# Kernel optimization log

Hardware: AMD Instinct MI355X
Metric: run time of the kernel (lower is better)

## Reference

```python
import jax, jax.numpy as jnp
import numpy as np

# Static config (matches init_kwargs); spatial shapes must be static for jit.
SPATIAL = [(96, 96), (48, 48), (24, 24), (12, 12)]  # (H_l, W_l)
D, NH, NL, NP = 256, 8, 4, 4
DH = D // NH
DFFN = 1024


def _ln(x, g, b):
    m = jnp.mean(x, -1, keepdims=True)
    v = jnp.var(x, -1, keepdims=True)
    return (x - m) * jax.lax.rsqrt(v + 1e-5) * g + b


def _bilinear_sample(v, loc, H, W):
    # v: (N, H*W, D) projected value for one level; loc: (N,Lq,NH,NP,2) in [0,1]
    # Matches grid_sample(align_corners=False, padding_mode='zeros'):
    # pixel coord = loc * size - 0.5, zero outside.
    N = v.shape[0]
    v = v.reshape(N, H, W, NH, DH)
    x = loc[..., 0] * W - 0.5
    y = loc[..., 1] * H - 0.5
    x0 = jnp.floor(x)
    y0 = jnp.floor(y)
    wx = x - x0
    wy = y - y0
    x0i = x0.astype(jnp.int32)
    y0i = y0.astype(jnp.int32)
    b = jnp.arange(N)[:, None, None, None]
    h = jnp.arange(NH)[None, None, :, None]

    def gather(yi, xi):
        valid = (yi >= 0) & (yi < H) & (xi >= 0) & (xi < W)
        s = v[b, jnp.clip(yi, 0, H - 1), jnp.clip(xi, 0, W - 1), h]  # (N,Lq,NH,NP,DH)
        return s * valid[..., None]

    s00 = gather(y0i, x0i)
    s01 = gather(y0i, x0i + 1)
    s10 = gather(y0i + 1, x0i)
    s11 = gather(y0i + 1, x0i + 1)
    return (s00 * ((1 - wy) * (1 - wx))[..., None]
            + s01 * ((1 - wy) * wx)[..., None]
            + s10 * (wy * (1 - wx))[..., None]
            + s11 * (wy * wx)[..., None])  # (N,Lq,NH,NP,DH)


def setup_inputs() -> dict:
    key = jax.random.key(0)
    ks = jax.random.split(key, 16)
    N, Lq = 8, 1024

    def nrm(k, shp, scale=1.0):
        return jax.random.normal(k, shp, dtype=jnp.float32) * scale

    return dict(
        tgt=nrm(ks[0], (N, Lq, D)),
        reference_points=jax.random.uniform(ks[1], (N, Lq, NL, 2), dtype=jnp.float32),
        src0=nrm(ks[2], (N, 96 * 96, 16)),
        src1=nrm(ks[3], (N, 48 * 48, 32)),
        src2=nrm(ks[4], (N, 24 * 24, 16)),
        src3=nrm(ks[5], (N, 12 * 12, 32)),
        Wv0=nrm(ks[6], (16, D), 0.25), bv0=jnp.zeros((D,), jnp.float32),
        Wv1=nrm(ks[7], (32, D), 0.18), bv1=jnp.zeros((D,), jnp.float32),
        Woff=nrm(ks[8], (D, NH * NL * NP * 2), 0.01), boff=nrm(ks[9], (NH * NL * NP * 2,), 0.5),
        Wattn=nrm(ks[10], (D, NH * NL * NP), 0.01), battn=jnp.zeros((NH * NL * NP,), jnp.float32),
        Wout=nrm(ks[11], (D, D), 1.0 / 16), bout=jnp.zeros((D,), jnp.float32),
        g1=jnp.ones((D,), jnp.float32), be1=jnp.zeros((D,), jnp.float32),
        W1=nrm(ks[12], (D, DFFN), 1.0 / 16), b1=jnp.zeros((DFFN,), jnp.float32),
        W2=nrm(ks[13], (DFFN, D), 1.0 / 32), b2=jnp.zeros((D,), jnp.float32),
        g3=jnp.ones((D,), jnp.float32), be3=jnp.zeros((D,), jnp.float32),
    )


def reference(tgt, reference_points, src0, src1, src2, src3,
              Wv0, bv0, Wv1, bv1, Woff, boff, Wattn, battn, Wout, bout,
              g1, be1, W1, b1, W2, b2, g3, be3):
    N, Lq, _ = tgt.shape
    # Per-level value projection (value_{idx % (n_levels//2)}: 16->D, 32->D cycling)
    values = [src0 @ Wv0 + bv0, src1 @ Wv1 + bv1, src2 @ Wv0 + bv0, src3 @ Wv1 + bv1]

    off = (tgt @ Woff + boff).reshape(N, Lq, NH, NL, NP, 2)
    attn = jax.nn.softmax((tgt @ Wattn + battn).reshape(N, Lq, NH, NL * NP), axis=-1)
    attn = attn.reshape(N, Lq, NH, NL, NP)

    # offset_normalizer = [W_l, H_l]
    norm = jnp.array([[w, h] for (h, w) in SPATIAL], dtype=tgt.dtype)  # (NL,2)
    loc = reference_points[:, :, None, :, None, :] + off / norm[None, None, None, :, None, :]

    sampled = jnp.stack(
        [_bilinear_sample(values[l], loc[:, :, :, l], SPATIAL[l][0], SPATIAL[l][1])
         for l in range(NL)], axis=3)  # (N,Lq,NH,NL,NP,DH)
    ms_out = jnp.sum(sampled * attn[..., None], axis=(3, 4)).reshape(N, Lq, D)
    ms_out = ms_out @ Wout + bout

    # decoder layer: residual + LN, FFN + residual + LN (dropout=0 / eval)
    t = _ln(tgt + ms_out, g1, be1)
    ff = jax.nn.relu(t @ W1 + b1) @ W2 + b2
    return _ln(t + ff, g3, be3)
```

## Files before the change

kernel.cpp:

```cpp
#include <hip/hip_runtime.h>
#include <math.h>


typedef __bf16 bf16x8 __attribute__((ext_vector_type(8)));
typedef float  f32x4  __attribute__((ext_vector_type(4)));
typedef unsigned short ushort8 __attribute__((ext_vector_type(8)));

#define VB0 0
#define VB1 18874368
#define VB2 23592960
#define VB3 24772608
#define VTOT 25067520

__device__ __forceinline__ unsigned short f2bf(float f) {
    unsigned u = __float_as_uint(f);
    u += 0x7FFF + ((u >> 16) & 1);
    return (unsigned short)(u >> 16);
}

__device__ __forceinline__ void gload16(const void* g, void* l) {
    __builtin_amdgcn_global_load_lds(
        (const __attribute__((address_space(1))) unsigned int*)g,
        (__attribute__((address_space(3))) unsigned int*)l, 16, 0, 0);
}

__global__ __launch_bounds__(256) void prep_kernel(
    const float* __restrict__ tgt, const float* __restrict__ Woff,
    const float* __restrict__ Wattn, const float* __restrict__ Wout,
    const float* __restrict__ W1, const float* __restrict__ W2,
    const float* __restrict__ boff, const float* __restrict__ battn,
    const float* __restrict__ Wv0, const float* __restrict__ Wv1,
    unsigned short* __restrict__ tgt_bf, unsigned short* __restrict__ Btoa,
    unsigned short* __restrict__ WoT, unsigned short* __restrict__ W1T,
    unsigned short* __restrict__ W2T, float* __restrict__ boa,
    unsigned short* __restrict__ WvT0, unsigned short* __restrict__ WvT1)
{
    __shared__ float sT[64][65];
    const int b = blockIdx.x, t = threadIdx.x;
    if (b < 2048) {
        const int i = (b * 256 + t) * 4;
        const float4 v = *(const float4*)&tgt[i];
        ushort4 o;
        o.x = f2bf(v.x); o.y = f2bf(v.y); o.z = f2bf(v.z); o.w = f2bf(v.w);
        *(ushort4*)&tgt_bf[i] = o;
        return;
    }
    if (b == 2048) {
        if (t < 384) boa[t] = (t < 256) ? boff[t] : battn[t - 256];
#pragma unroll
        for (int k = 0; k < 16; ++k) {
            WvT0[t * 32 + k]      = f2bf(Wv0[k * 256 + t]);
            WvT0[t * 32 + 16 + k] = 0;
        }
#pragma unroll
        for (int k = 0; k < 32; ++k)
            WvT1[t * 32 + k] = f2bf(Wv1[k * 256 + t]);
        return;
    }
    int tb = b - 2049;
    const float* src; unsigned short* dst; int srcN, dstK, tn, tk;
    if (tb < 16)       { src = Woff;  dst = Btoa;          srcN = 256;  dstK = 256;  tn = tb >> 2; tk = tb & 3; }
    else if (tb < 24)  { tb -= 16; src = Wattn; dst = Btoa + 65536; srcN = 128; dstK = 256; tn = tb >> 2; tk = tb & 3; }
    else if (tb < 40)  { tb -= 24; src = Wout;  dst = WoT; srcN = 256;  dstK = 256;  tn = tb >> 2; tk = tb & 3; }
    else if (tb < 104) { tb -= 40; src = W1;    dst = W1T; srcN = 1024; dstK = 256;  tn = tb >> 2; tk = tb & 3; }
    else               { tb -= 104; src = W2;   dst = W2T; srcN = 256;  dstK = 1024; tn = tb >> 4; tk = tb & 15; }
    const int n0 = tn * 64, k0 = tk * 64;
    const int j = t & 63, i0 = t >> 6;
#pragma unroll
    for (int s = 0; s < 16; ++s) {
        const int i = i0 + s * 4;
        sT[i][j] = src[(size_t)(k0 + i) * srcN + n0 + j];
    }
    __syncthreads();
#pragma unroll
    for (int s = 0; s < 16; ++s) {
        const int nr = i0 + s * 4;
        dst[(size_t)(n0 + nr) * dstK + k0 + j] = f2bf(sT[j][nr]);
    }
}

template <int BM, int BN, int RELU, int OUTBF16>
__global__ __launch_bounds__(256) void gemm_bf16(
    const unsigned short* __restrict__ A, const unsigned short* __restrict__ Bt,
    const float* __restrict__ bias, float* __restrict__ C32,
    unsigned short* __restrict__ C16, int M, int N, int K)
{
    constexpr int MF = BM / 32, NF = BN / 32;
    constexpr int CA = BM / 16, CB = BN / 16;
    constexpr int CPW = (CA + CB) / 4;

    __shared__ unsigned short As[2][BM * 32];
    __shared__ unsigned short Bs[2][BN * 32];

    const int t = threadIdx.x, wv = t >> 6, l = t & 63;
    const int m0 = blockIdx.y * BM, n0 = blockIdx.x * BN;
    const int wm = wv >> 1, wn = wv & 1;
    const int lr = l >> 2, sl = l & 3;
    const int swsl = sl ^ ((lr >> 1) & 3);
    const int fr = l & 15, kg = l >> 4;
    const int rsw = (fr >> 1) & 3;

    f32x4 acc[MF][NF];
#pragma unroll
    for (int i = 0; i < MF; ++i)
#pragma unroll
        for (int j = 0; j < NF; ++j) acc[i][j] = (f32x4){0.f, 0.f, 0.f, 0.f};

#define STAGE(bufi, k0)                                                        \
    do {                                                                       \
        _Pragma("unroll")                                                      \
        for (int cc = 0; cc < CPW; ++cc) {                                     \
            const int ch = wv * CPW + cc;                                      \
            if (ch < CA) {                                                     \
                gload16(A + (size_t)(m0 + ch * 16 + lr) * K + (k0) + swsl * 8, \
                        &As[bufi][ch * 512]);                                  \
            } else {                                                           \
                const int cb2 = ch - CA;                                       \
                gload16(Bt + (size_t)(n0 + cb2 * 16 + lr) * K + (k0) + swsl * 8,\
                        &Bs[bufi][cb2 * 512]);                                 \
            }                                                                  \
        }                                                                      \
    } while (0)

    const int NT = K >> 5;
    STAGE(0, 0);
    asm volatile("s_waitcnt vmcnt(0)" ::: "memory");
    __syncthreads();

    for (int tt = 0; tt < NT; ++tt) {
        const int cur = tt & 1;
        if (tt + 1 < NT) STAGE(cur ^ 1, (tt + 1) * 32);

        bf16x8 af[MF], bfr[NF];
#pragma unroll
        for (int i = 0; i < MF; ++i)
            af[i] = *(const bf16x8*)&As[cur][(wm * (MF * 16) + i * 16 + fr) * 32 + (kg ^ rsw) * 8];
#pragma unroll
        for (int j = 0; j < NF; ++j)
            bfr[j] = *(const bf16x8*)&Bs[cur][(wn * (NF * 16) + j * 16 + fr) * 32 + (kg ^ rsw) * 8];
#pragma unroll
        for (int i = 0; i < MF; ++i)
#pragma unroll
            for (int j = 0; j < NF; ++j)
                acc[i][j] = __builtin_amdgcn_mfma_f32_16x16x32_bf16(af[i], bfr[j], acc[i][j], 0, 0, 0);

        asm volatile("s_waitcnt vmcnt(0)" ::: "memory");
        __syncthreads();
    }
#undef STAGE

    const int q4 = (l >> 4) * 4;
#pragma unroll
    for (int j = 0; j < NF; ++j) {
        const int col = n0 + wn * (NF * 16) + j * 16 + fr;
        const float bj = bias[col];
#pragma unroll
        for (int i = 0; i < MF; ++i) {
#pragma unroll
            for (int r = 0; r < 4; ++r) {
                const int row = m0 + wm * (MF * 16) + i * 16 + q4 + r;
                float v = acc[i][j][r] + bj;
                if (RELU) v = fmaxf(v, 0.f);
                if (OUTBF16) C16[(size_t)row * N + col] = f2bf(v);
                else         C32[(size_t)row * N + col] = v;
            }
        }
    }
}

__global__ __launch_bounds__(256) void vproj_gemm(
    const float* __restrict__ src0, const float* __restrict__ src1,
    const float* __restrict__ src2, const float* __restrict__ src3,
    const unsigned short* __restrict__ WvT0, const unsigned short* __restrict__ WvT1,
    const float* __restrict__ bv0, const float* __restrict__ bv1,
    unsigned short* __restrict__ vals)
{
    __shared__ unsigned short As[128 * 32];
    __shared__ unsigned short Bs[128 * 32];

    const int ly = blockIdx.y;
    const float* A32; const unsigned short* Bt; const float* bias;
    size_t ob; int lm, Kr;
    if (ly < 576)      { A32 = src0; Bt = WvT0; bias = bv0; ob = VB0; lm = ly;       Kr = 16; }
    else if (ly < 720) { A32 = src1; Bt = WvT1; bias = bv1; ob = VB1; lm = ly - 576; Kr = 32; }
    else if (ly < 756) { A32 = src2; Bt = WvT0; bias = bv0; ob = VB2; lm = ly - 720; Kr = 16; }
    else               { A32 = src3; Bt = WvT1; bias = bv1; ob = VB3; lm = ly - 756; Kr = 32; }

    const int t = threadIdx.x, wv = t >> 6, l = t & 63;
    const int m0 = lm * 128, n0 = blockIdx.x * 128;
    const int wm = wv >> 1, wn = wv & 1;
    const int lr = l >> 2, sl = l & 3;
    const int swsl = sl ^ ((lr >> 1) & 3);
    const int fr = l & 15, kg = l >> 4;
    const int rsw = (fr >> 1) & 3;

#pragma unroll
    for (int cc = 0; cc < 2; ++cc) {
        const int ch = wv * 2 + cc;
        gload16(Bt + (size_t)(n0 + ch * 16 + lr) * 32 + swsl * 8, &Bs[ch * 512]);
    }

    {
        const int r = t >> 1, hh = t & 1;
        const int rs = (r >> 1) & 3;
        if (Kr == 32) {
            const float4* sp = (const float4*)(A32 + (size_t)(m0 + r) * 32 + hh * 16);
            const float4 a0 = sp[0], a1 = sp[1], a2 = sp[2], a3 = sp[3];
            ushort8 w0, w1;
            w0[0] = f2bf(a0.x); w0[1] = f2bf(a0.y); w0[2] = f2bf(a0.z); w0[3] = f2bf(a0.w);
            w0[4] = f2bf(a1.x); w0[5] = f2bf(a1.y); w0[6] = f2bf(a1.z); w0[7] = f2bf(a1.w);
            w1[0] = f2bf(a2.x); w1[1] = f2bf(a2.y); w1[2] = f2bf(a2.z); w1[3] = f2bf(a2.w);
            w1[4] = f2bf(a3.x); w1[5] = f2bf(a3.y); w1[6] = f2bf(a3.z); w1[7] = f2bf(a3.w);
            *(ushort8*)&As[r * 32 + ((hh * 2 + 0) ^ rs) * 8] = w0;
            *(ushort8*)&As[r * 32 + ((hh * 2 + 1) ^ rs) * 8] = w1;
        } else {
            if (hh == 0) {
                const float4* sp = (const float4*)(A32 + (size_t)(m0 + r) * 16);
                const float4 a0 = sp[0], a1 = sp[1], a2 = sp[2], a3 = sp[3];
                ushort8 w0, w1;
                w0[0] = f2bf(a0.x); w0[1] = f2bf(a0.y); w0[2] = f2bf(a0.z); w0[3] = f2bf(a0.w);
                w0[4] = f2bf(a1.x); w0[5] = f2bf(a1.y); w0[6] = f2bf(a1.z); w0[7] = f2bf(a1.w);
                w1[0] = f2bf(a2.x); w1[1] = f2bf(a2.y); w1[2] = f2bf(a2.z); w1[3] = f2bf(a2.w);
                w1[4] = f2bf(a3.x); w1[5] = f2bf(a3.y); w1[6] = f2bf(a3.z); w1[7] = f2bf(a3.w);
                *(ushort8*)&As[r * 32 + ((0) ^ rs) * 8] = w0;
                *(ushort8*)&As[r * 32 + ((1) ^ rs) * 8] = w1;
            } else {
                const ushort8 z = {0, 0, 0, 0, 0, 0, 0, 0};
                *(ushort8*)&As[r * 32 + ((2) ^ rs) * 8] = z;
                *(ushort8*)&As[r * 32 + ((3) ^ rs) * 8] = z;
            }
        }
    }
    asm volatile("s_waitcnt vmcnt(0)" ::: "memory");
    __syncthreads();

    f32x4 acc[4][4];
#pragma unroll
    for (int i = 0; i < 4; ++i)
#pragma unroll
        for (int j = 0; j < 4; ++j) acc[i][j] = (f32x4){0.f, 0.f, 0.f, 0.f};

    bf16x8 af[4], bfr[4];
#pragma unroll
    for (int i = 0; i < 4; ++i)
        af[i] = *(const bf16x8*)&As[(wm * 64 + i * 16 + fr) * 32 + (kg ^ rsw) * 8];
#pragma unroll
    for (int j = 0; j < 4; ++j)
        bfr[j] = *(const bf16x8*)&Bs[(wn * 64 + j * 16 + fr) * 32 + (kg ^ rsw) * 8];
#pragma unroll
    for (int i = 0; i < 4; ++i)
#pragma unroll
        for (int j = 0; j < 4; ++j)
            acc[i][j] = __builtin_amdgcn_mfma_f32_16x16x32_bf16(af[i], bfr[j], acc[i][j], 0, 0, 0);

    const int q4 = (l >> 4) * 4;
#pragma unroll
    for (int j = 0; j < 4; ++j) {
        const int col = n0 + wn * 64 + j * 16 + fr;
        const float bj = bias[col];
#pragma unroll
        for (int i = 0; i < 4; ++i) {
#pragma unroll
            for (int r = 0; r < 4; ++r) {
                const int row = m0 + wm * 64 + i * 16 + q4 + r;
                vals[ob + (size_t)row * 256 + col] = f2bf(acc[i][j][r] + bj);
            }
        }
    }
}

__device__ __forceinline__ void acc8(const unsigned short* p, float w, float* a)
{
    const uint4 u = *(const uint4*)p;
    a[0] = fmaf(w, __uint_as_float(u.x << 16), a[0]);
    a[1] = fmaf(w, __uint_as_float(u.x & 0xffff0000u), a[1]);
    a[2] = fmaf(w, __uint_as_float(u.y << 16), a[2]);
    a[3] = fmaf(w, __uint_as_float(u.y & 0xffff0000u), a[3]);
    a[4] = fmaf(w, __uint_as_float(u.z << 16), a[4]);
    a[5] = fmaf(w, __uint_as_float(u.z & 0xffff0000u), a[5]);
    a[6] = fmaf(w, __uint_as_float(u.w << 16), a[6]);
    a[7] = fmaf(w, __uint_as_float(u.w & 0xffff0000u), a[7]);
}

__global__ __launch_bounds__(256) void sampler_kernel(
    const unsigned short* __restrict__ vals, const float* __restrict__ offlog,
    const float* __restrict__ ref, unsigned short* __restrict__ msout)
{
    __shared__ float sOff[8][256];
    __shared__ float sLog[8][128];
    __shared__ float sRef[8][8];

    const int t = threadIdx.x, w = t >> 6, l = t & 63;
    const int qbase = blockIdx.x * 8;

    for (int j = l; j < 768; j += 64) {
        const int second = (j >= 384);
        const int lq = w * 2 + second;
        const int jj = second ? j - 384 : j;
        const float v = offlog[(size_t)(qbase + lq) * 384 + jj];
        if (jj < 256) {
            const int h = jj >> 5, r = jj & 31;
            sOff[lq][(r >> 1) * 16 + h * 2 + (r & 1)] = v;
        } else {
            const int j2 = jj - 256;
            sLog[lq][(j2 & 15) * 8 + (j2 >> 4)] = v;
        }
    }
    if (l < 16)
        sRef[w * 2 + (l >> 3)][l & 7] = ref[(size_t)(qbase + w * 2 + (l >> 3)) * 8 + (l & 7)];
    __syncthreads();

    const int lq = w * 2 + (l >> 5);
    const int b  = qbase + lq;
    const int n  = b >> 10;
    const int h  = (l >> 2) & 7;
    const int lg = l & 3;

    float mx = -1e30f;
#pragma unroll
    for (int i = 0; i < 16; ++i) mx = fmaxf(mx, sLog[lq][i * 8 + h]);
    float e[16], s = 0.f;
#pragma unroll
    for (int i = 0; i < 16; ++i) { e[i] = __expf(sLog[lq][i * 8 + h] - mx); s += e[i]; }
    const float inv = 1.f / s;

    float acc[8] = {0.f, 0.f, 0.f, 0.f, 0.f, 0.f, 0.f, 0.f};
    const int dims[4] = {96, 48, 24, 12};
    const int hwsz[4] = {9216, 2304, 576, 144};
    const size_t vbase[4] = {VB0, VB1, VB2, VB3};

#pragma unroll
    for (int lv = 0; lv < 4; ++lv) {
        const int W = dims[lv];
        const float fx = sRef[lq][lv * 2]     * (float)W - 0.5f;
        const float fy = sRef[lq][lv * 2 + 1] * (float)W - 0.5f;
        const unsigned short* vb =
            vals + vbase[lv] + (size_t)n * hwsz[lv] * 256 + h * 32 + lg * 8;
#pragma unroll
        for (int p = 0; p < 4; ++p) {
            const float2 xy = *(const float2*)&sOff[lq][((lv * 4 + p) * 8 + h) * 2];
            const float x = fx + xy.x;
            const float y = fy + xy.y;
            const float x0f = floorf(x), y0f = floorf(y);
            const float wx = x - x0f, wy = y - y0f;
            const int x0 = (int)x0f, y0 = (int)y0f;
            const float aw = e[lv * 4 + p] * inv;
            const float vx0 = ((unsigned)x0       < (unsigned)W) ? 1.f - wx : 0.f;
            const float vx1 = ((unsigned)(x0 + 1) < (unsigned)W) ? wx       : 0.f;
            const float vy0 = ((unsigned)y0       < (unsigned)W) ? 1.f - wy : 0.f;
            const float vy1 = ((unsigned)(y0 + 1) < (unsigned)W) ? wy       : 0.f;
            const int cx0 = min(max(x0, 0), W - 1);
            const int cx1 = min(max(x0 + 1, 0), W - 1);
            const int cy0 = min(max(y0, 0), W - 1) * W;
            const int cy1 = min(max(y0 + 1, 0), W - 1) * W;
            acc8(vb + (size_t)(cy0 + cx0) * 256, aw * vy0 * vx0, acc);
            acc8(vb + (size_t)(cy0 + cx1) * 256, aw * vy0 * vx1, acc);
            acc8(vb + (size_t)(cy1 + cx0) * 256, aw * vy1 * vx0, acc);
            acc8(vb + (size_t)(cy1 + cx1) * 256, aw * vy1 * vx1, acc);
        }
    }
    uint4 o;
    o.x = (unsigned)f2bf(acc[0]) | ((unsigned)f2bf(acc[1]) << 16);
    o.y = (unsigned)f2bf(acc[2]) | ((unsigned)f2bf(acc[3]) << 16);
    o.z = (unsigned)f2bf(acc[4]) | ((unsigned)f2bf(acc[5]) << 16);
    o.w = (unsigned)f2bf(acc[6]) | ((unsigned)f2bf(acc[7]) << 16);
    *(uint4*)&msout[(size_t)b * 256 + h * 32 + lg * 8] = o;
}

__global__ __launch_bounds__(256) void ln_kernel(
    const float* __restrict__ a, const float* __restrict__ b,
    const float* __restrict__ g, const float* __restrict__ be,
    float* __restrict__ out32, unsigned short* __restrict__ out16)
{
    const int t = threadIdx.x, w = t >> 6, l = t & 63;
    const int row = blockIdx.x * 4 + w;
    const size_t base = (size_t)row * 256 + l * 4;
    const float4 av = *(const float4*)&a[base];
    const float4 bv = *(const float4*)&b[base];
    const float x0 = av.x + bv.x, x1 = av.y + bv.y, x2 = av.z + bv.z, x3 = av.w + bv.w;
    float s  = x0 + x1 + x2 + x3;
    float s2 = x0 * x0 + x1 * x1 + x2 * x2 + x3 * x3;
#pragma unroll
    for (int o = 32; o; o >>= 1) { s += __shfl_xor(s, o); s2 += __shfl_xor(s2, o); }
    const float mean = s * (1.f / 256.f);
    const float rstd = rsqrtf(s2 * (1.f / 256.f) - mean * mean + 1e-5f);
    const float4 gv = *(const float4*)&g[l * 4];
    const float4 ev = *(const float4*)&be[l * 4];
    const float y0 = (x0 - mean) * rstd * gv.x + ev.x;
    const float y1 = (x1 - mean) * rstd * gv.y + ev.y;
    const float y2 = (x2 - mean) * rstd * gv.z + ev.z;
    const float y3 = (x3 - mean) * rstd * gv.w + ev.w;
    float4 o4; o4.x = y0; o4.y = y1; o4.z = y2; o4.w = y3;
    *(float4*)&out32[base] = o4;
    if (out16) {
        ushort4 o;
        o.x = f2bf(y0); o.y = f2bf(y1); o.z = f2bf(y2); o.w = f2bf(y3);
        *(ushort4*)&out16[base] = o;
    }
}

extern "C" void kernel_launch(void* const* d_in, const int* in_sizes, int n_in,
                              void* d_out, int out_size, void* d_ws, size_t ws_size,
                              hipStream_t stream)
{
    const float* tgt   = (const float*)d_in[0];
    const float* ref   = (const float*)d_in[1];
    const float* src0  = (const float*)d_in[2];
    const float* src1  = (const float*)d_in[3];
    const float* src2  = (const float*)d_in[4];
    const float* src3  = (const float*)d_in[5];
    const float* Wv0   = (const float*)d_in[6];
    const float* bv0   = (const float*)d_in[7];
    const float* Wv1   = (const float*)d_in[8];
    const float* bv1   = (const float*)d_in[9];
    const float* Woff  = (const float*)d_in[10];
    const float* boff  = (const float*)d_in[11];
    const float* Wattn = (const float*)d_in[12];
    const float* battn = (const float*)d_in[13];
    const float* Wout  = (const float*)d_in[14];
    const float* bout  = (const float*)d_in[15];
    const float* g1    = (const float*)d_in[16];
    const float* be1   = (const float*)d_in[17];
    const float* W1    = (const float*)d_in[18];
    const float* b1    = (const float*)d_in[19];
    const float* W2    = (const float*)d_in[20];
    const float* b2    = (const float*)d_in[21];
    const float* g3    = (const float*)d_in[22];
    const float* be3   = (const float*)d_in[23];

    char* w8 = (char*)d_ws;
    unsigned short* vals_bf  = (unsigned short*)(w8 + 0);
    unsigned short* tgt_bf   = (unsigned short*)(w8 + 50135040);
    unsigned short* Btoa     = (unsigned short*)(w8 + 54329344);
    unsigned short* WoT      = (unsigned short*)(w8 + 54525952);
    unsigned short* W1T      = (unsigned short*)(w8 + 54657024);
    unsigned short* W2T      = (unsigned short*)(w8 + 55181312);
    unsigned short* ffn1_bf  = (unsigned short*)(w8 + 55705600);
    unsigned short* msout_bf = (unsigned short*)(w8 + 72482816);
    unsigned short* tbuf16   = (unsigned short*)(w8 + 76677120);
    float* boa    = (float*)(w8 + 80871424);
    float* offlog = (float*)(w8 + 80872960);
    float* ms2    = (float*)(w8 + 93455872);
    float* tbuf32 = (float*)(w8 + 101844480);
    float* ffn2   = (float*)(w8 + 110233088);
    unsigned short* WvT0  = (unsigned short*)(w8 + 93455872 + 6266880);
    unsigned short* WvT1  = (unsigned short*)(w8 + 93455872 + 6283264);

    const dim3 blk(256);

    prep_kernel<<<2217, blk, 0, stream>>>(tgt, Woff, Wattn, Wout, W1, W2, boff, battn,
                                          Wv0, Wv1,
                                          tgt_bf, Btoa, WoT, W1T, W2T, boa, WvT0, WvT1);

    vproj_gemm<<<dim3(2, 765), blk, 0, stream>>>(src0, src1, src2, src3,
                                                 WvT0, WvT1, bv0, bv1, vals_bf);

    gemm_bf16<64, 128, 0, 0><<<dim3(3, 128), blk, 0, stream>>>(
        tgt_bf, Btoa, boa, offlog, (unsigned short*)nullptr, 8192, 384, 256);
    sampler_kernel<<<1024, blk, 0, stream>>>(vals_bf, offlog, ref, msout_bf);

    gemm_bf16<64, 128, 0, 0><<<dim3(2, 128), blk, 0, stream>>>(
        msout_bf, WoT, bout, ms2, (unsigned short*)nullptr, 8192, 256, 256);
    ln_kernel<<<2048, blk, 0, stream>>>(tgt, ms2, g1, be1, tbuf32, tbuf16);

    gemm_bf16<128, 128, 1, 1><<<dim3(8, 64), blk, 0, stream>>>(
        tbuf16, W1T, b1, (float*)nullptr, ffn1_bf, 8192, 1024, 256);
    gemm_bf16<64, 128, 0, 0><<<dim3(2, 128), blk, 0, stream>>>(
        ffn1_bf, W2T, b2, ffn2, (unsigned short*)nullptr, 8192, 256, 1024);
    ln_kernel<<<2048, blk, 0, stream>>>(tbuf32, ffn2, g3, be3, (float*)d_out,
                                        (unsigned short*)nullptr);
}
```

Measured before the change: 207.9 us.

## Fuse output and FFN2 GEMMs with residual-add LayerNorm epilogue

Adds a gemm_ln kernel where each block computes a full 32x256 output row tile, adds bias and residual, and performs LayerNorm in the epilogue using shuffles plus a small shared reduction across waves. It replaces the two GEMM+ln_kernel pairs, removing the fp32 intermediate round trips and two launches. The cost is only 256 blocks with 32-row tiles and a simple double buffer with full waits, which may underuse the machine compared with the earlier tilings.

```diff
diff --git a/kernel.cpp b/kernel.cpp
--- a/kernel.cpp
+++ b/kernel.cpp
@@ -168,6 +168,131 @@
     }
 }
 
+template <int OUT16>
+__global__ __launch_bounds__(256) void gemm_ln(
+    const unsigned short* __restrict__ A, const unsigned short* __restrict__ Bt,
+    const float* __restrict__ bias, const float* __restrict__ resid,
+    const float* __restrict__ g, const float* __restrict__ be,
+    float* __restrict__ out32, unsigned short* __restrict__ out16,
+    int M, int K)
+{
+    __shared__ unsigned short As[2][32 * 32];
+    __shared__ unsigned short Bs[2][256 * 32];
+    __shared__ float sLN[4][32][2];
+
+    const int t = threadIdx.x, wv = t >> 6, l = t & 63;
+    const int m0 = blockIdx.x * 32;
+    const int wn = wv;
+    const int lr = l >> 2, sl = l & 3;
+    const int swsl = sl ^ ((lr >> 1) & 3);
+    const int fr = l & 15, kg = l >> 4;
+    const int rsw = (fr >> 1) & 3;
+
+    f32x4 acc[2][4];
+#pragma unroll
+    for (int i = 0; i < 2; ++i)
+#pragma unroll
+        for (int j = 0; j < 4; ++j) acc[i][j] = (f32x4){0.f, 0.f, 0.f, 0.f};
+
+#define STAGE_LN(bufi, k0)                                                     \
+    for (int ch = wv; ch < 18; ch += 4) {                                      \
+        if (ch < 2) {                                                          \
+            gload16(A + (size_t)(m0 + ch * 16 + lr) * K + (k0) + swsl * 8,     \
+                    &As[bufi][ch * 512]);                                      \
+        } else {                                                               \
+            gload16(Bt + (size_t)((ch - 2) * 16 + lr) * K + (k0) + swsl * 8,   \
+                    &Bs[bufi][(ch - 2) * 512]);                                \
+        }                                                                      \
+    }
+
+    const int NT = K >> 5;
+    STAGE_LN(0, 0);
+    asm volatile("s_waitcnt vmcnt(0)" ::: "memory");
+    __syncthreads();
+
+    for (int tt = 0; tt < NT; ++tt) {
+        const int cur = tt & 1;
+        if (tt + 1 < NT) { STAGE_LN(cur ^ 1, (tt + 1) * 32); }
+
+        bf16x8 af[2], bfr[4];
+#pragma unroll
+        for (int i = 0; i < 2; ++i)
+            af[i] = *(const bf16x8*)&As[cur][(i * 16 + fr) * 32 + (kg ^ rsw) * 8];
+#pragma unroll
+        for (int j = 0; j < 4; ++j)
+            bfr[j] = *(const bf16x8*)&Bs[cur][(wn * 64 + j * 16 + fr) * 32 + (kg ^ rsw) * 8];
+#pragma unroll
+        for (int i = 0; i < 2; ++i)
+#pragma unroll
+            for (int j = 0; j < 4; ++j)
+                acc[i][j] = __builtin_amdgcn_mfma_f32_16x16x32_bf16(af[i], bfr[j], acc[i][j], 0, 0, 0);
+
+        asm volatile("s_waitcnt vmcnt(0)" ::: "memory");
+        __syncthreads();
+    }
+#undef STAGE_LN
+
+    const int q4 = kg * 4;
+    float bj[4];
+#pragma unroll
+    for (int j = 0; j < 4; ++j) bj[j] = bias[wn * 64 + j * 16 + fr];
+
+    float s[2][4] = {}, q[2][4] = {};
+#pragma unroll
+    for (int i = 0; i < 2; ++i)
+#pragma unroll
+        for (int r = 0; r < 4; ++r) {
+            const int row = m0 + i * 16 + q4 + r;
+#pragma unroll
+            for (int j = 0; j < 4; ++j) {
+                const int col = wn * 64 + j * 16 + fr;
+                float v = acc[i][j][r] + bj[j] + resid[(size_t)row * 256 + col];
+                acc[i][j][r] = v;
+                s[i][r] += v;
+                q[i][r] += v * v;
+            }
+        }
+#pragma unroll
+    for (int o = 1; o < 16; o <<= 1) {
+#pragma unroll
+        for (int i = 0; i < 2; ++i)
+#pragma unroll
+            for (int r = 0; r < 4; ++r) {
+                s[i][r] += __shfl_xor(s[i][r], o);
+                q[i][r] += __shfl_xor(q[i][r], o);
+            }
+    }
+    if (fr == 0) {
+#pragma unroll
+        for (int i = 0; i < 2; ++i)
+#pragma unroll
+            for (int r = 0; r < 4; ++r) {
+                sLN[wn][i * 16 + q4 + r][0] = s[i][r];
+                sLN[wn][i * 16 + q4 + r][1] = q[i][r];
+            }
+    }
+    __syncthreads();
+
+#pragma unroll
+    for (int i = 0; i < 2; ++i)
+#pragma unroll
+        for (int r = 0; r < 4; ++r) {
+            const int rloc = i * 16 + q4 + r;
+            const float S = sLN[0][rloc][0] + sLN[1][rloc][0] + sLN[2][rloc][0] + sLN[3][rloc][0];
+            const float Q = sLN[0][rloc][1] + sLN[1][rloc][1] + sLN[2][rloc][1] + sLN[3][rloc][1];
+            const float mean = S * (1.f / 256.f);
+            const float rstd = rsqrtf(Q * (1.f / 256.f) - mean * mean + 1e-5f);
+            const int row = m0 + rloc;
+#pragma unroll
+            for (int j = 0; j < 4; ++j) {
+                const int col = wn * 64 + j * 16 + fr;
+                const float y = (acc[i][j][r] - mean) * rstd * g[col] + be[col];
+                out32[(size_t)row * 256 + col] = y;
+                if (OUT16) out16[(size_t)row * 256 + col] = f2bf(y);
+            }
+        }
+}
+
 __global__ __launch_bounds__(256) void vproj_gemm(
     const float* __restrict__ src0, const float* __restrict__ src1,
     const float* __restrict__ src2, const float* __restrict__ src3,
@@ -199,7 +324,6 @@
         const int ch = wv * 2 + cc;
         gload16(Bt + (size_t)(n0 + ch * 16 + lr) * 32 + swsl * 8, &Bs[ch * 512]);
     }
-
     {
         const int r = t >> 1, hh = t & 1;
         const int rs = (r >> 1) & 3;
@@ -367,38 +491,6 @@
     *(uint4*)&msout[(size_t)b * 256 + h * 32 + lg * 8] = o;
 }
 
-__global__ __launch_bounds__(256) void ln_kernel(
-    const float* __restrict__ a, const float* __restrict__ b,
-    const float* __restrict__ g, const float* __restrict__ be,
-    float* __restrict__ out32, unsigned short* __restrict__ out16)
-{
-    const int t = threadIdx.x, w = t >> 6, l = t & 63;
-    const int row = blockIdx.x * 4 + w;
-    const size_t base = (size_t)row * 256 + l * 4;
-    const float4 av = *(const float4*)&a[base];
-    const float4 bv = *(const float4*)&b[base];
-    const float x0 = av.x + bv.x, x1 = av.y + bv.y, x2 = av.z + bv.z, x3 = av.w + bv.w;
-    float s  = x0 + x1 + x2 + x3;
-    float s2 = x0 * x0 + x1 * x1 + x2 * x2 + x3 * x3;
-#pragma unroll
-    for (int o = 32; o; o >>= 1) { s += __shfl_xor(s, o); s2 += __shfl_xor(s2, o); }
-    const float mean = s * (1.f / 256.f);
-    const float rstd = rsqrtf(s2 * (1.f / 256.f) - mean * mean + 1e-5f);
-    const float4 gv = *(const float4*)&g[l * 4];
-    const float4 ev = *(const float4*)&be[l * 4];
-    const float y0 = (x0 - mean) * rstd * gv.x + ev.x;
-    const float y1 = (x1 - mean) * rstd * gv.y + ev.y;
-    const float y2 = (x2 - mean) * rstd * gv.z + ev.z;
-    const float y3 = (x3 - mean) * rstd * gv.w + ev.w;
-    float4 o4; o4.x = y0; o4.y = y1; o4.z = y2; o4.w = y3;
-    *(float4*)&out32[base] = o4;
-    if (out16) {
-        ushort4 o;
-        o.x = f2bf(y0); o.y = f2bf(y1); o.z = f2bf(y2); o.w = f2bf(y3);
-        *(ushort4*)&out16[base] = o;
-    }
-}
-
 extern "C" void kernel_launch(void* const* d_in, const int* in_sizes, int n_in,
                               void* d_out, int out_size, void* d_ws, size_t ws_size,
                               hipStream_t stream)
@@ -440,9 +532,7 @@
     unsigned short* tbuf16   = (unsigned short*)(w8 + 76677120);
     float* boa    = (float*)(w8 + 80871424);
     float* offlog = (float*)(w8 + 80872960);
-    float* ms2    = (float*)(w8 + 93455872);
     float* tbuf32 = (float*)(w8 + 101844480);
-    float* ffn2   = (float*)(w8 + 110233088);
     unsigned short* WvT0  = (unsigned short*)(w8 + 93455872 + 6266880);
     unsigned short* WvT1  = (unsigned short*)(w8 + 93455872 + 6283264);
 
@@ -459,14 +549,12 @@
         tgt_bf, Btoa, boa, offlog, (unsigned short*)nullptr, 8192, 384, 256);
     sampler_kernel<<<1024, blk, 0, stream>>>(vals_bf, offlog, ref, msout_bf);
 
-    gemm_bf16<64, 128, 0, 0><<<dim3(2, 128), blk, 0, stream>>>(
-        msout_bf, WoT, bout, ms2, (unsigned short*)nullptr, 8192, 256, 256);
-    ln_kernel<<<2048, blk, 0, stream>>>(tgt, ms2, g1, be1, tbuf32, tbuf16);
+    gemm_ln<1><<<256, blk, 0, stream>>>(msout_bf, WoT, bout, tgt, g1, be1,
+                                        tbuf32, tbuf16, 8192, 256);
 
     gemm_bf16<128, 128, 1, 1><<<dim3(8, 64), blk, 0, stream>>>(
         tbuf16, W1T, b1, (float*)nullptr, ffn1_bf, 8192, 1024, 256);
-    gemm_bf16<64, 128, 0, 0><<<dim3(2, 128), blk, 0, stream>>>(
-        ffn1_bf, W2T, b2, ffn2, (unsigned short*)nullptr, 8192, 256, 1024);
-    ln_kernel<<<2048, blk, 0, stream>>>(tbuf32, ffn2, g3, be3, (float*)d_out,
-                                        (unsigned short*)nullptr);
-}
+
+    gemm_ln<0><<<256, blk, 0, stream>>>(ffn1_bf, W2T, b2, tbuf32, g3, be3,
+                                        (float*)d_out, (unsigned short*)nullptr, 8192, 1024);
+}
```

New measurement: 213.1 us. 1.02x slower.
